# Performance work log

Measured on AMD Instinct MI355X. Metric: run time of the kernel, lower is better.

The kernel has to match this reference:

```python
import jax, jax.numpy as jnp
import numpy as np

H = 16  # n_heads

def setup_inputs() -> dict:
    key = jax.random.key(0)
    ks = jax.random.split(key, 7)
    B, L, D = 4, 2048, 1024
    s = 0.02
    return {
        "z": jax.random.normal(ks[0], (B, L, D), jnp.float32),
        "connection": jax.random.normal(ks[1], (B, L, D), jnp.float32),
        "Wq": jax.random.normal(ks[2], (2 * D, D), jnp.float32) * s,
        "Wk": jax.random.normal(ks[3], (2 * D, D), jnp.float32) * s,
        "Wv": jax.random.normal(ks[4], (D, D), jnp.float32) * s,
        "Wo": jax.random.normal(ks[5], (D, D), jnp.float32) * s,
        "temp": jnp.float32(1.0),
    }

def reference(z, connection, Wq, Wk, Wv, Wo, temp):
    B, L, D = z.shape
    hd = D // H
    zc = jnp.concatenate([z, connection], axis=-1)          # [B,L,2D]
    Q = (zc @ Wq).reshape(B, L, H, hd).transpose(0, 2, 1, 3)  # [B,H,L,hd]
    K = (zc @ Wk).reshape(B, L, H, hd).transpose(0, 2, 1, 3)
    V = (z @ Wv).reshape(B, L, H, hd).transpose(0, 2, 1, 3)
    scale = (hd ** -0.5) * temp
    scores = jnp.einsum('bhqd,bhkd->bhqk', Q, K) * scale     # [B,H,L,L]
    rel = jax.nn.sigmoid(scores)
    rel_sum = jnp.clip(rel.sum(-1, keepdims=True), 1.0, None)
    out = jnp.einsum('bhqk,bhkd->bhqd', rel, V) / rel_sum
    out = out.transpose(0, 2, 1, 3).reshape(B, L, D)
    return out @ Wo
```

## Files before the change

kernel.cpp:

```cpp
#include <hip/hip_runtime.h>

typedef unsigned short u16;
typedef unsigned int u32;
typedef __bf16 bf16x8 __attribute__((ext_vector_type(8)));
typedef float f32x4 __attribute__((ext_vector_type(4)));

#define DEV static __device__ __forceinline__

DEV void gload16(const void* g, void* l) {
    __builtin_amdgcn_global_load_lds(
        (const __attribute__((address_space(1))) void*)g,
        (__attribute__((address_space(3))) void*)l, 16, 0, 0);
}

DEV void store_c(float* p, float v) { *p = v; }
DEV void store_c(u16* p, float v) { *(__bf16*)p = (__bf16)v; }

DEV int swz(int row, int bytecol) { return row * 128 + (bytecol ^ ((row & 7) << 4)); }
DEV int swzP(int row, int bytecol) {
    return row * 128 + (bytecol ^ ((row & 7) << 4) ^ (row & 8));
}

DEV void xcd_remap(int& bx, int& by, int gx, int gy) {
    int nwg = gx * gy;
    int bid = by * gx + bx;
    int logical = (bid & 7) * (nwg >> 3) + (bid >> 3);
    bx = logical % gx;
    by = logical / gx;
}

__global__ void pack_zc(const float* __restrict__ z, const float* __restrict__ cn,
                        u16* __restrict__ zc) {
    size_t i = ((size_t)blockIdx.x * blockDim.x + threadIdx.x) * 4;
    size_t t = i >> 11;
    int c = (int)(i & 2047);
    const float* src = (c < 1024) ? (z + t * 1024 + c) : (cn + t * 1024 + (c - 1024));
    float4 v = *reinterpret_cast<const float4*>(src);
    union { __bf16 h[4]; uint2 u; } o;
    o.h[0] = (__bf16)v.x; o.h[1] = (__bf16)v.y;
    o.h[2] = (__bf16)v.z; o.h[3] = (__bf16)v.w;
    *reinterpret_cast<uint2*>(zc + i) = o.u;
}

__global__ void transpose_conv_w(const float* __restrict__ W, u16* __restrict__ WT,
                                 int K, int N, const float* __restrict__ scl) {
    __shared__ float tile[32][33];
    float sc = scl ? scl[0] * 0.18033688011112042f : 1.0f;
    int n0 = blockIdx.x * 32, k0 = blockIdx.y * 32;
    int tx = threadIdx.x, ty = threadIdx.y;
    #pragma unroll
    for (int i = ty; i < 32; i += 8)
        tile[i][tx] = W[(size_t)(k0 + i) * N + n0 + tx];
    __syncthreads();
    #pragma unroll
    for (int i = ty; i < 32; i += 8)
        *(__bf16*)&WT[(size_t)(n0 + i) * K + k0 + tx] = (__bf16)(tile[tx][i] * sc);
}

__global__ void transpose_v(const u16* __restrict__ Vf, u16* __restrict__ Vt) {
    __shared__ u16 tile[32][33];
    int bh = blockIdx.z; int b = bh >> 4, h = bh & 15;
    int l0 = blockIdx.x * 32, d0 = blockIdx.y * 32;
    int tx = threadIdx.x, ty = threadIdx.y;
    #pragma unroll
    for (int i = ty; i < 32; i += 8)
        tile[i][tx] = Vf[(size_t)(b * 2048 + l0 + i) * 1024 + h * 64 + d0 + tx];
    __syncthreads();
    #pragma unroll
    for (int i = ty; i < 32; i += 8)
        Vt[((size_t)bh * 64 + d0 + i) * 2048 + l0 + tx] = tile[tx][i];
}

template <typename OutT>
__global__ __launch_bounds__(256, 2)
void gemm_bt(const u16* __restrict__ A, const u16* __restrict__ BT,
             OutT* __restrict__ C, int M, int N, int K,
             int lda, int ldb, int ldc) {
    __shared__ u16 As[128 * 64];
    __shared__ u16 Bs[128 * 64];
    const int tid = threadIdx.x;
    const int lane = tid & 63;
    const int wid = tid >> 6;
    int bx = blockIdx.x, by = blockIdx.y;
    xcd_remap(bx, by, gridDim.x, gridDim.y);
    const int m0 = bx * 128;
    const int n0 = by * 128;
    const int wr = (wid >> 1) * 64;
    const int wc = (wid & 1) * 64;

    f32x4 acc[4][4];
    #pragma unroll
    for (int i = 0; i < 4; ++i)
        #pragma unroll
        for (int j = 0; j < 4; ++j)
            acc[i][j] = f32x4{0.f, 0.f, 0.f, 0.f};

    const int srcoff = ((lane & 7) ^ (lane >> 3)) * 8;
    const int rb = wid * 32 + (lane >> 3);
    const u16* aptr[4]; const u16* bptr[4];
    #pragma unroll
    for (int p = 0; p < 4; ++p) {
        aptr[p] = A  + (size_t)(m0 + rb + p * 8) * lda + srcoff;
        bptr[p] = BT + (size_t)(n0 + rb + p * 8) * ldb + srcoff;
    }

    for (int k0 = 0; k0 < K; k0 += 64) {
        __syncthreads();
        #pragma unroll
        for (int p = 0; p < 4; ++p)
            gload16(aptr[p] + k0, (char*)As + (wid * 4 + p) * 1024);
        #pragma unroll
        for (int p = 0; p < 4; ++p)
            gload16(bptr[p] + k0, (char*)Bs + (wid * 4 + p) * 1024);
        __syncthreads();

        #pragma unroll
        for (int kk = 0; kk < 64; kk += 32) {
            bf16x8 af[4], bfr[4];
            #pragma unroll
            for (int i = 0; i < 4; ++i) {
                int row = wr + i * 16 + (lane & 15);
                af[i] = *reinterpret_cast<const bf16x8*>(
                    reinterpret_cast<const char*>(As) + swz(row, (kk + (lane >> 4) * 8) * 2));
            }
            #pragma unroll
            for (int j = 0; j < 4; ++j) {
                int row = wc + j * 16 + (lane & 15);
                bfr[j] = *reinterpret_cast<const bf16x8*>(
                    reinterpret_cast<const char*>(Bs) + swz(row, (kk + (lane >> 4) * 8) * 2));
            }
            #pragma unroll
            for (int i = 0; i < 4; ++i)
                #pragma unroll
                for (int j = 0; j < 4; ++j)
                    acc[i][j] = __builtin_amdgcn_mfma_f32_16x16x32_bf16(af[i], bfr[j], acc[i][j], 0, 0, 0);
        }
    }

    #pragma unroll
    for (int i = 0; i < 4; ++i)
        #pragma unroll
        for (int j = 0; j < 4; ++j)
            #pragma unroll
            for (int r = 0; r < 4; ++r) {
                int row = m0 + wr + i * 16 + (lane >> 4) * 4 + r;
                int col = n0 + wc + j * 16 + (lane & 15);
                store_c(&C[(size_t)row * ldc + col], acc[i][j][r]);
            }
}

template <typename OutT>
__global__ __launch_bounds__(512, 2)
void gemm8_bt(const u16* __restrict__ A, const u16* __restrict__ BT,
              OutT* __restrict__ C, int M, int N, int K,
              int lda, int ldb, int ldc) {
    __shared__ u16 As[2][256 * 64];
    __shared__ u16 Bs[2][256 * 64];
    const int tid = threadIdx.x;
    const int lane = tid & 63;
    const int wid = tid >> 6;
    const int wm = wid >> 2;
    const int wn = wid & 3;
    const int hi = lane >> 4;
    const int lq = lane & 15;
    int bx = blockIdx.x, by = blockIdx.y;
    xcd_remap(bx, by, gridDim.x, gridDim.y);
    const int m0 = bx * 256;
    const int n0 = by * 256;

    f32x4 acc[8][4];
    #pragma unroll
    for (int i = 0; i < 8; ++i)
        #pragma unroll
        for (int j = 0; j < 4; ++j)
            acc[i][j] = f32x4{0.f, 0.f, 0.f, 0.f};

    const int srcoff = ((lane & 7) ^ (lane >> 3)) * 8;
    const int rb = wid * 32 + (lane >> 3);
    const u16* aptr[4]; const u16* bptr[4];
    #pragma unroll
    for (int p = 0; p < 4; ++p) {
        aptr[p] = A  + (size_t)(m0 + rb + p * 8) * lda + srcoff;
        bptr[p] = BT + (size_t)(n0 + rb + p * 8) * ldb + srcoff;
    }

    const int nt = K >> 6;

    #pragma unroll
    for (int p = 0; p < 4; ++p) gload16(aptr[p], (char*)As[0] + (wid * 4 + p) * 1024);
    #pragma unroll
    for (int p = 0; p < 4; ++p) gload16(bptr[p], (char*)Bs[0] + (wid * 4 + p) * 1024);
    #pragma unroll
    for (int p = 0; p < 4; ++p) gload16(aptr[p] + 64, (char*)As[1] + (wid * 4 + p) * 1024);
    #pragma unroll
    for (int p = 0; p < 4; ++p) gload16(bptr[p] + 64, (char*)Bs[1] + (wid * 4 + p) * 1024);
    asm volatile("s_waitcnt vmcnt(8)" ::: "memory");
    __builtin_amdgcn_s_barrier();
    __builtin_amdgcn_sched_barrier(0);

    int cur = 0;
    for (int t = 0; t < nt; ++t) {
        #pragma unroll
        for (int q = 0; q < 4; ++q) {
            const int mq = q >> 1, nq = q & 1;
            bf16x8 af[4][2], bfr[2][2];
            #pragma unroll
            for (int kx = 0; kx < 2; ++kx) {
                #pragma unroll
                for (int mi = 0; mi < 4; ++mi) {
                    int row = wm * 128 + mq * 64 + mi * 16 + lq;
                    af[mi][kx] = *reinterpret_cast<const bf16x8*>(
                        reinterpret_cast<const char*>(As[cur]) + swz(row, kx * 64 + hi * 16));
                }
                #pragma unroll
                for (int ni = 0; ni < 2; ++ni) {
                    int row = wn * 64 + nq * 32 + ni * 16 + lq;
                    bfr[ni][kx] = *reinterpret_cast<const bf16x8*>(
                        reinterpret_cast<const char*>(Bs[cur]) + swz(row, kx * 64 + hi * 16));
                }
            }
            __builtin_amdgcn_s_setprio(1);
            #pragma unroll
            for (int kx = 0; kx < 2; ++kx)
                #pragma unroll
                for (int mi = 0; mi < 4; ++mi)
                    #pragma unroll
                    for (int ni = 0; ni < 2; ++ni)
                        acc[mq * 4 + mi][nq * 2 + ni] = __builtin_amdgcn_mfma_f32_16x16x32_bf16(
                            af[mi][kx], bfr[ni][kx], acc[mq * 4 + mi][nq * 2 + ni], 0, 0, 0);
            __builtin_amdgcn_s_setprio(0);
            __builtin_amdgcn_s_barrier();
        }
        __builtin_amdgcn_sched_barrier(0);
        if (t + 2 < nt) {
            const int k0n = (t + 2) * 64;
            #pragma unroll
            for (int p = 0; p < 4; ++p) gload16(aptr[p] + k0n, (char*)As[cur] + (wid * 4 + p) * 1024);
            #pragma unroll
            for (int p = 0; p < 4; ++p) gload16(bptr[p] + k0n, (char*)Bs[cur] + (wid * 4 + p) * 1024);
            asm volatile("s_waitcnt vmcnt(8)" ::: "memory");
            __builtin_amdgcn_s_barrier();
        } else if (t + 1 < nt) {
            asm volatile("s_waitcnt vmcnt(0)" ::: "memory");
            __builtin_amdgcn_s_barrier();
        }
        __builtin_amdgcn_sched_barrier(0);
        cur ^= 1;
    }

    #pragma unroll
    for (int am = 0; am < 8; ++am)
        #pragma unroll
        for (int an = 0; an < 4; ++an)
            #pragma unroll
            for (int r = 0; r < 4; ++r) {
                int row = m0 + wm * 128 + (am >> 2) * 64 + (am & 3) * 16 + hi * 4 + r;
                int col = n0 + wn * 64 + (an >> 1) * 32 + (an & 1) * 16 + lq;
                store_c(&C[(size_t)row * ldc + col], acc[am][an][r]);
            }
}

__global__ __launch_bounds__(256, 2)
void attn_kernel(const u16* __restrict__ QKf, const u16* __restrict__ Vt,
                 u16* __restrict__ Oa) {
    constexpr int L = 2048, D = 1024, QKLD = 2048, HD = 64;
    __shared__ u16 Ks[2][64 * 64];
    __shared__ u16 Vs[2][64 * 64];
    __shared__ u16 Ps[4][32 * 64];

    const int tid = threadIdx.x;
    const int lane = tid & 63;
    const int wid = tid >> 6;
    const int hi = lane >> 4;
    const int lq = lane & 15;
    int bx = blockIdx.x, by = blockIdx.y;
    xcd_remap(bx, by, gridDim.x, gridDim.y);
    const int bh = by;
    const int b = bh >> 4, h = bh & 15;
    const int q0 = bx * 128;

    const u16* Qbase = QKf + (size_t)(b * L) * QKLD + h * HD;
    const u16* Kbase = Qbase + 1024;
    const u16* Vbase = Vt + (size_t)bh * HD * L;

    const int srcoff = ((lane & 7) ^ (lane >> 3)) * 8;
    const int rb = wid * 16 + (lane >> 3);
    const u16* kptr[2]; const u16* vptr[2];
    #pragma unroll
    for (int p = 0; p < 2; ++p) {
        kptr[p] = Kbase + (size_t)(rb + p * 8) * QKLD + srcoff;
        vptr[p] = Vbase + (size_t)(rb + p * 8) * L + srcoff;
    }

    bf16x8 qf[2][2];
    #pragma unroll
    for (int i = 0; i < 2; ++i)
        #pragma unroll
        for (int kx = 0; kx < 2; ++kx)
            qf[i][kx] = *reinterpret_cast<const bf16x8*>(
                Qbase + (size_t)(q0 + wid * 32 + i * 16 + lq) * QKLD + kx * 32 + hi * 8);

    #pragma unroll
    for (int p = 0; p < 2; ++p)
        gload16(kptr[p], (char*)Ks[0] + (wid * 2 + p) * 1024);
    #pragma unroll
    for (int p = 0; p < 2; ++p)
        gload16(vptr[p], (char*)Vs[0] + (wid * 2 + p) * 1024);

    bf16x8 onesf;
    #pragma unroll
    for (int j = 0; j < 8; ++j) onesf[j] = (__bf16)1.0f;

    f32x4 oacc[4][2];
    #pragma unroll
    for (int ct = 0; ct < 4; ++ct)
        #pragma unroll
        for (int i = 0; i < 2; ++i) oacc[ct][i] = f32x4{0.f, 0.f, 0.f, 0.f};
    f32x4 racc[2];
    racc[0] = f32x4{0.f, 0.f, 0.f, 0.f};
    racc[1] = f32x4{0.f, 0.f, 0.f, 0.f};

    __syncthreads();
    int cur = 0;

    for (int k0 = 0; k0 < L; k0 += 64) {
        if (k0 + 64 < L) {
            #pragma unroll
            for (int p = 0; p < 2; ++p)
                gload16(kptr[p] + (size_t)(k0 + 64) * QKLD, (char*)Ks[cur ^ 1] + (wid * 2 + p) * 1024);
            #pragma unroll
            for (int p = 0; p < 2; ++p)
                gload16(vptr[p] + (k0 + 64), (char*)Vs[cur ^ 1] + (wid * 2 + p) * 1024);
        }

        f32x4 s[4][2];
        #pragma unroll
        for (int ct = 0; ct < 4; ++ct)
            #pragma unroll
            for (int i = 0; i < 2; ++i) s[ct][i] = f32x4{0.f, 0.f, 0.f, 0.f};
        #pragma unroll
        for (int kx = 0; kx < 2; ++kx) {
            bf16x8 ak[4];
            #pragma unroll
            for (int ct = 0; ct < 4; ++ct) {
                int krow = ct * 16 + lq;
                ak[ct] = *reinterpret_cast<const bf16x8*>(
                    reinterpret_cast<const char*>(Ks[cur]) + swz(krow, kx * 64 + hi * 16));
            }
            #pragma unroll
            for (int ct = 0; ct < 4; ++ct)
                #pragma unroll
                for (int i = 0; i < 2; ++i)
                    s[ct][i] = __builtin_amdgcn_mfma_f32_16x16x32_bf16(ak[ct], qf[i][kx], s[ct][i], 0, 0, 0);
        }

        #pragma unroll
        for (int i = 0; i < 2; ++i) {
            int prow = i * 16 + lq;
            #pragma unroll
            for (int ct = 0; ct < 4; ++ct) {
                float t0 = 1.0f + __builtin_amdgcn_exp2f(-s[ct][i][0]);
                float t1 = 1.0f + __builtin_amdgcn_exp2f(-s[ct][i][1]);
                float t2 = 1.0f + __builtin_amdgcn_exp2f(-s[ct][i][2]);
                float t3 = 1.0f + __builtin_amdgcn_exp2f(-s[ct][i][3]);
                float m01 = t0 * t1, m23 = t2 * t3;
                float rall = __builtin_amdgcn_rcpf(m01 * m23);
                float r01 = m23 * rall, r23 = m01 * rall;
                union { __bf16 hh[4]; uint2 uu; } pk;
                pk.hh[0] = (__bf16)(t1 * r01);
                pk.hh[1] = (__bf16)(t0 * r01);
                pk.hh[2] = (__bf16)(t3 * r23);
                pk.hh[3] = (__bf16)(t2 * r23);
                *reinterpret_cast<uint2*>(reinterpret_cast<char*>(Ps[wid]) +
                    swzP(prow, ct * 32 + hi * 8)) = pk.uu;
            }
        }

        #pragma unroll
        for (int kx = 0; kx < 2; ++kx) {
            bf16x8 ap[2];
            #pragma unroll
            for (int i = 0; i < 2; ++i) {
                int prow = i * 16 + lq;
                union { u32 w[4]; bf16x8 v; } apu;
                *reinterpret_cast<uint2*>(&apu.w[0]) = *reinterpret_cast<const uint2*>(
                    reinterpret_cast<const char*>(Ps[wid]) + swzP(prow, kx * 64 + hi * 16));
                *reinterpret_cast<uint2*>(&apu.w[2]) = *reinterpret_cast<const uint2*>(
                    reinterpret_cast<const char*>(Ps[wid]) + swzP(prow, kx * 64 + hi * 16 + 8));
                ap[i] = apu.v;
            }
            racc[0] = __builtin_amdgcn_mfma_f32_16x16x32_bf16(ap[0], onesf, racc[0], 0, 0, 0);
            racc[1] = __builtin_amdgcn_mfma_f32_16x16x32_bf16(ap[1], onesf, racc[1], 0, 0, 0);
            #pragma unroll
            for (int ct = 0; ct < 4; ++ct) {
                int vrow = ct * 16 + lq;
                bf16x8 bv = *reinterpret_cast<const bf16x8*>(
                    reinterpret_cast<const char*>(Vs[cur]) + swz(vrow, kx * 64 + hi * 16));
                #pragma unroll
                for (int i = 0; i < 2; ++i)
                    oacc[ct][i] = __builtin_amdgcn_mfma_f32_16x16x32_bf16(ap[i], bv, oacc[ct][i], 0, 0, 0);
            }
        }

        __syncthreads();
        cur ^= 1;
    }

    float rdiv[2][4];
    #pragma unroll
    for (int i = 0; i < 2; ++i)
        #pragma unroll
        for (int r = 0; r < 4; ++r)
            rdiv[i][r] = __builtin_amdgcn_rcpf(fmaxf(racc[i][r], 1.0f));

    #pragma unroll
    for (int ct = 0; ct < 4; ++ct)
        #pragma unroll
        for (int i = 0; i < 2; ++i)
            #pragma unroll
            for (int r = 0; r < 4; ++r) {
                int row = q0 + wid * 32 + i * 16 + hi * 4 + r;
                int col = h * HD + ct * 16 + lq;
                *(__bf16*)&Oa[(size_t)(b * L + row) * D + col] =
                    (__bf16)(oacc[ct][i][r] * rdiv[i][r]);
            }
}

extern "C" void kernel_launch(void* const* d_in, const int* in_sizes, int n_in,
                              void* d_out, int out_size, void* d_ws, size_t ws_size,
                              hipStream_t stream) {
    const float* z    = (const float*)d_in[0];
    const float* cn   = (const float*)d_in[1];
    const float* Wq   = (const float*)d_in[2];
    const float* Wk   = (const float*)d_in[3];
    const float* Wv   = (const float*)d_in[4];
    const float* Wo   = (const float*)d_in[5];
    const float* temp = (const float*)d_in[6];

    char* ws = (char*)d_ws;
    u16* zc  = (u16*)ws; ws += (size_t)8192 * 2048 * 2;
    u16* WqT = (u16*)ws; ws += (size_t)1024 * 2048 * 2;
    u16* WkT = (u16*)ws; ws += (size_t)1024 * 2048 * 2;
    u16* WvT = (u16*)ws; ws += (size_t)1024 * 1024 * 2;
    u16* WoT = (u16*)ws; ws += (size_t)1024 * 1024 * 2;
    u16* QKf = (u16*)ws; ws += (size_t)8192 * 2048 * 2;
    u16* Vf  = (u16*)ws; ws += (size_t)8192 * 1024 * 2;
    u16* Vt  = zc;
    u16* Oa  = Vf;

    pack_zc<<<16384, 256, 0, stream>>>(z, cn, zc);

    dim3 tb(32, 8);
    transpose_conv_w<<<dim3(32, 64), tb, 0, stream>>>(Wq, WqT, 2048, 1024, temp);
    transpose_conv_w<<<dim3(32, 64), tb, 0, stream>>>(Wk, WkT, 2048, 1024, nullptr);
    transpose_conv_w<<<dim3(32, 32), tb, 0, stream>>>(Wv, WvT, 1024, 1024, nullptr);
    transpose_conv_w<<<dim3(32, 32), tb, 0, stream>>>(Wo, WoT, 1024, 1024, nullptr);

    gemm8_bt<u16><<<dim3(32, 8), 512, 0, stream>>>(zc, WqT, QKf, 8192, 2048, 2048, 2048, 2048, 2048);
    gemm_bt<u16><<<dim3(64, 8), 256, 0, stream>>>(zc, WvT, Vf, 8192, 1024, 1024, 2048, 1024, 1024);

    transpose_v<<<dim3(64, 2, 64), tb, 0, stream>>>(Vf, Vt);

    attn_kernel<<<dim3(16, 64), 256, 0, stream>>>(QKf, Vt, Oa);

    gemm_bt<float><<<dim3(64, 8), 256, 0, stream>>>(Oa, WoT, (float*)d_out, 8192, 1024, 1024, 1024, 1024, 1024);
}
```

Baseline: 395.9 us.

## Single-buffer V tile in attention, raise occupancy, and merge weight transposes

The attention kernel now keeps a single V buffer in LDS. It loads V for the current tile at the start of each iteration and waits on it with an explicit vmcnt after the sigmoid stage, which frees shared memory. Launch bounds rise from 2 to 4 blocks per CU to improve latency hiding. The four weight transpose launches are merged into one kernel that picks its matrix from blockIdx.y, saving launch overhead. The V load is now exposed within each iteration, and the higher occupancy target may force register spills.

Result: no change. 400.5 us (+1.2%).

```diff
diff --git a/kernel.cpp b/kernel.cpp
--- a/kernel.cpp
+++ b/kernel.cpp
@@ -42,11 +42,20 @@
     *reinterpret_cast<uint2*>(zc + i) = o.u;
 }
 
-__global__ void transpose_conv_w(const float* __restrict__ W, u16* __restrict__ WT,
-                                 int K, int N, const float* __restrict__ scl) {
+__global__ void transpose_conv_w_all(const float* __restrict__ Wq, const float* __restrict__ Wk,
+                                     const float* __restrict__ Wv, const float* __restrict__ Wo,
+                                     u16* __restrict__ WqT, u16* __restrict__ WkT,
+                                     u16* __restrict__ WvT, u16* __restrict__ WoT,
+                                     const float* __restrict__ temp) {
     __shared__ float tile[32][33];
-    float sc = scl ? scl[0] * 0.18033688011112042f : 1.0f;
-    int n0 = blockIdx.x * 32, k0 = blockIdx.y * 32;
+    int zone = blockIdx.y;
+    const float* W; u16* WT; int K; float sc = 1.0f;
+    if (zone < 64)       { W = Wq; WT = WqT; K = 2048; sc = temp[0] * 0.18033688011112042f; }
+    else if (zone < 128) { W = Wk; WT = WkT; K = 2048; zone -= 64; }
+    else if (zone < 160) { W = Wv; WT = WvT; K = 1024; zone -= 128; }
+    else                 { W = Wo; WT = WoT; K = 1024; zone -= 160; }
+    const int N = 1024;
+    int n0 = blockIdx.x * 32, k0 = zone * 32;
     int tx = threadIdx.x, ty = threadIdx.y;
     #pragma unroll
     for (int i = ty; i < 32; i += 8)
@@ -260,12 +269,12 @@
             }
 }
 
-__global__ __launch_bounds__(256, 2)
+__global__ __launch_bounds__(256, 4)
 void attn_kernel(const u16* __restrict__ QKf, const u16* __restrict__ Vt,
                  u16* __restrict__ Oa) {
     constexpr int L = 2048, D = 1024, QKLD = 2048, HD = 64;
     __shared__ u16 Ks[2][64 * 64];
-    __shared__ u16 Vs[2][64 * 64];
+    __shared__ u16 Vs[64 * 64];
     __shared__ u16 Ps[4][32 * 64];
 
     const int tid = threadIdx.x;
@@ -303,9 +312,6 @@
     #pragma unroll
     for (int p = 0; p < 2; ++p)
         gload16(kptr[p], (char*)Ks[0] + (wid * 2 + p) * 1024);
-    #pragma unroll
-    for (int p = 0; p < 2; ++p)
-        gload16(vptr[p], (char*)Vs[0] + (wid * 2 + p) * 1024);
 
     bf16x8 onesf;
     #pragma unroll
@@ -324,13 +330,14 @@
     int cur = 0;
 
     for (int k0 = 0; k0 < L; k0 += 64) {
-        if (k0 + 64 < L) {
+        #pragma unroll
+        for (int p = 0; p < 2; ++p)
+            gload16(vptr[p] + k0, (char*)Vs + (wid * 2 + p) * 1024);
+        const bool more = (k0 + 64 < L);
+        if (more) {
             #pragma unroll
             for (int p = 0; p < 2; ++p)
                 gload16(kptr[p] + (size_t)(k0 + 64) * QKLD, (char*)Ks[cur ^ 1] + (wid * 2 + p) * 1024);
-            #pragma unroll
-            for (int p = 0; p < 2; ++p)
-                gload16(vptr[p] + (k0 + 64), (char*)Vs[cur ^ 1] + (wid * 2 + p) * 1024);
         }
 
         f32x4 s[4][2];
@@ -376,6 +383,10 @@
             }
         }
 
+        if (more) asm volatile("s_waitcnt vmcnt(2)" ::: "memory");
+        else      asm volatile("s_waitcnt vmcnt(0)" ::: "memory");
+        __builtin_amdgcn_sched_barrier(0);
+
         #pragma unroll
         for (int kx = 0; kx < 2; ++kx) {
             bf16x8 ap[2];
@@ -395,7 +406,7 @@
             for (int ct = 0; ct < 4; ++ct) {
                 int vrow = ct * 16 + lq;
                 bf16x8 bv = *reinterpret_cast<const bf16x8*>(
-                    reinterpret_cast<const char*>(Vs[cur]) + swz(vrow, kx * 64 + hi * 16));
+                    reinterpret_cast<const char*>(Vs) + swz(vrow, kx * 64 + hi * 16));
                 #pragma unroll
                 for (int i = 0; i < 2; ++i)
                     oacc[ct][i] = __builtin_amdgcn_mfma_f32_16x16x32_bf16(ap[i], bv, oacc[ct][i], 0, 0, 0);
@@ -451,10 +462,8 @@
     pack_zc<<<16384, 256, 0, stream>>>(z, cn, zc);
 
     dim3 tb(32, 8);
-    transpose_conv_w<<<dim3(32, 64), tb, 0, stream>>>(Wq, WqT, 2048, 1024, temp);
-    transpose_conv_w<<<dim3(32, 64), tb, 0, stream>>>(Wk, WkT, 2048, 1024, nullptr);
-    transpose_conv_w<<<dim3(32, 32), tb, 0, stream>>>(Wv, WvT, 1024, 1024, nullptr);
-    transpose_conv_w<<<dim3(32, 32), tb, 0, stream>>>(Wo, WoT, 1024, 1024, nullptr);
+    transpose_conv_w_all<<<dim3(32, 192), tb, 0, stream>>>(
+        Wq, Wk, Wv, Wo, WqT, WkT, WvT, WoT, temp);
 
     gemm8_bt<u16><<<dim3(32, 8), 512, 0, stream>>>(zc, WqT, QKf, 8192, 2048, 2048, 2048, 2048, 2048);
     gemm_bt<u16><<<dim3(64, 8), 256, 0, stream>>>(zc, WvT, Vf, 8192, 1024, 1024, 2048, 1024, 1024);
```
